# Kernel optimization log

Measured on AMD Instinct MI355X. Metric: run time of the kernel, lower is better.

Reference implementation:

```python
import jax, jax.numpy as jnp
import numpy as np

L_IN, L_K = 1, 1            # degree ranges (0..L)
C_IN, K_CH, H = 16, 8, 4    # in_channels, k_channels (per head), num_heads
C_OUT = H * K_CH            # 32
E, N_NODES, EMB = 32768, 4096, 64
M_IN, M_K = (L_IN + 1) ** 2, (L_K + 1) ** 2


def _so2_pairs(L_in, L_out):
    # enumerate SO(2)-equivariant weight blocks: for each order m, all (l_in, l_out)
    # pairs with l >= m; m=0 uses 1 matrix, m>0 uses 2 (real/imag parts).
    pairs, w = [], 0
    for m in range(min(L_in, L_out) + 1):
        for l_in in range(m, L_in + 1):
            for l_out in range(m, L_out + 1):
                pairs.append((m, l_in, l_out, w))
                w += 1 if m == 0 else 2
    return pairs, w

_PAIRS, NUM_W = _so2_pairs(L_IN, L_K)  # NUM_W = 6 for L_in=L_k=1


def so2_linear(x, W, L_in, L_out):
    # x: [E, (L_in+1)^2, Cin]; W: [NUM_W, Cin, Cout] (shared) or [E, NUM_W, Cin, Cout] (per-edge)
    per_edge = (W.ndim == 4)
    Cout = W.shape[-1]
    out = jnp.zeros((x.shape[0], (L_out + 1) ** 2, Cout), x.dtype)

    def mat(xs, w):
        return jnp.einsum('ec,eco->eo', xs, W[:, w]) if per_edge else xs @ W[w]

    pairs, _ = _so2_pairs(L_in, L_out)
    for m, l_in, l_out, w in pairs:
        i_in, i_out = l_in * (l_in + 1), l_out * (l_out + 1)  # flat index of (l, m=0)
        if m == 0:
            out = out.at[:, i_out].add(mat(x[:, i_in], w))
        else:
            xp, xn = x[:, i_in + m], x[:, i_in - m]
            out = out.at[:, i_out + m].add(mat(xp, w) - mat(xn, w + 1))
            out = out.at[:, i_out - m].add(mat(xp, w + 1) + mat(xn, w))
    return out


def segment_softmax(z, index, num_segments):
    # PyG-style softmax over ragged neighborhoods (max is detached, as in PyG)
    zmax = jax.lax.stop_gradient(jax.ops.segment_max(z, index, num_segments=num_segments))
    e = jnp.exp(z - zmax[index])
    denom = jax.ops.segment_sum(e, index, num_segments=num_segments)
    return e / denom[index]


def setup_inputs() -> dict:
    key = jax.random.key(0)
    ks = jax.random.split(key, 6)
    x_q = jax.random.normal(ks[0], (E, M_IN, C_IN), jnp.float32)
    x_k = jax.random.normal(ks[1], (E, M_IN, C_IN), jnp.float32)
    edge_emb = jax.random.normal(ks[2], (E, EMB), jnp.float32)
    index = jnp.sort(jax.random.randint(ks[3], (E,), 0, N_NODES))
    W_q = jax.random.normal(ks[4], (NUM_W, C_IN, C_OUT), jnp.float32) / np.sqrt(C_IN)
    W_p = jax.random.normal(ks[5], (EMB, NUM_W * C_IN * C_OUT), jnp.float32) / np.sqrt(EMB)
    return {"x_q": x_q, "x_k": x_k, "edge_emb": edge_emb, "index": index,
            "W_q": W_q, "W_p": W_p, "num_nodes": N_NODES}


def reference(x_q, x_k, edge_emb, index, W_q, W_p, num_nodes):
    # q_ij = W_Q x_i ; static SO2 weights
    q = so2_linear(x_q, W_q, L_IN, L_K).reshape(-1, M_K, H, K_CH)
    # k_ij = W_K(||r_ij||) x_j ; per-edge dynamic SO2 weights from edge embedding
    W_k = (edge_emb @ W_p).reshape(-1, NUM_W, C_IN, C_OUT)
    k = so2_linear(x_k, W_k, L_IN, L_K).reshape(-1, M_K, H, K_CH)
    scale = (K_CH // H) ** (-0.5)  # faithful to original: (k_channels // num_heads)**-0.5
    z = (q * k).sum((-1, -3)) * scale  # [E, H]
    return segment_softmax(z, index, num_nodes)
```

## Files before the change

### kernel.cpp

```cpp
#include <hip/hip_runtime.h>
#include <math.h>

#define E_TOTAL 32768
#define NUM_NODES 4096
#define SCALE 0.70710678118654752f

typedef __attribute__((ext_vector_type(8))) short bfrag;
typedef __attribute__((ext_vector_type(16))) float facc;

__device__ inline unsigned short f2bf(float f) {
  unsigned int u = __float_as_uint(f);
  unsigned int r = (u + 0x7FFFu + ((u >> 16) & 1u)) >> 16;
  return (unsigned short)r;
}
__device__ inline float bf2f(unsigned short s) {
  return __uint_as_float(((unsigned int)s) << 16);
}
__device__ inline void cvt8(const float* v, bfrag& hi, bfrag& lo) {
#pragma unroll
  for (int i = 0; i < 8; ++i) {
    unsigned short h = f2bf(v[i]);
    hi[i] = (short)h;
    lo[i] = (short)f2bf(v[i] - bf2f(h));
  }
}

__global__ __launch_bounds__(256) void prep_kernel(
    const float* __restrict__ Wp, const float* __restrict__ Wq,
    const int* __restrict__ index,
    unsigned short* __restrict__ fragWp, unsigned short* __restrict__ fragWq,
    int* __restrict__ offs)
{
  const int b = blockIdx.x, t = threadIdx.x;
  if (b < 96) {
    __shared__ unsigned short lds[4096];
    const int c = b / 6, w = b - c * 6;
    const int colbase = w * 512 + c * 32;
    const int cl = t & 31, dg = t >> 5;
#pragma unroll
    for (int i = 0; i < 8; ++i) {
      const int d = dg * 8 + i;
      const float v = Wp[(size_t)d * 3072 + colbase + cl];
      const unsigned short hi = f2bf(v);
      const unsigned short lo = f2bf(v - bf2f(hi));
      const int ks = d >> 4;
      const int lane = ((d >> 3) & 1) * 32 + cl;
      const int j = d & 7;
      lds[(ks * 2 + 0) * 512 + lane * 8 + j] = hi;
      lds[(ks * 2 + 1) * 512 + lane * 8 + j] = lo;
    }
    __syncthreads();
    unsigned short* dst = fragWp + (size_t)b * 4096;
    ((uint4*)dst)[t] = ((const uint4*)lds)[t];
    ((uint4*)dst)[t + 256] = ((const uint4*)lds)[t + 256];
  } else if (b < 103) {
    const int slot = b - 96;
    const int w = (slot == 6) ? 5 : slot;
    const float sgn = (slot == 6) ? -1.f : 1.f;
    for (int tt = t; tt < 512; tt += 256) {
      const int lane = tt >> 3, j = tt & 7;
      const int o = lane & 31, c = (lane >> 5) * 8 + j;
      const float v = sgn * Wq[(size_t)(w * 16 + c) * 32 + o];
      const unsigned short hi = f2bf(v);
      const unsigned short lo = f2bf(v - bf2f(hi));
      fragWq[slot * 1024 + lane * 8 + j] = hi;
      fragWq[slot * 1024 + 512 + lane * 8 + j] = lo;
    }
  } else {
    const int tg = (b - 103) * 256 + t;
    if (tg >= E_TOTAL) return;
    const int cur = index[tg];
    const int prev = (tg == 0) ? -1 : index[tg - 1];
    for (int n = prev + 1; n <= cur; ++n) offs[n] = tg;
    if (tg == E_TOTAL - 1)
      for (int n = cur + 1; n <= NUM_NODES; ++n) offs[n] = E_TOTAL;
  }
}

__global__ __launch_bounds__(256, 2) void main_kernel(
    const float* __restrict__ x_q, const float* __restrict__ x_k,
    const float* __restrict__ emb,
    const unsigned short* __restrict__ fragWp,
    const unsigned short* __restrict__ fragWq,
    float* __restrict__ z)
{
  __shared__ float xk_t[64][33];
  __shared__ float zred[4][32][4];

  const int t = threadIdx.x;
  const int lane = t & 63, wv = t >> 6;
  const int pr = wv & 1, ch = wv >> 1;
  const int col = lane & 31, half = lane >> 5;
  const int eb = blockIdx.x * 32;
  const int e = eb + col;

  {
    const int er = t >> 3, dq = (t & 7) * 8;
    const float* src = x_k + (size_t)(eb + er) * 64 + dq;
    float4 v0 = *(const float4*)(src);
    float4 v1 = *(const float4*)(src + 4);
    xk_t[dq + 0][er] = v0.x; xk_t[dq + 1][er] = v0.y;
    xk_t[dq + 2][er] = v0.z; xk_t[dq + 3][er] = v0.w;
    xk_t[dq + 4][er] = v1.x; xk_t[dq + 5][er] = v1.y;
    xk_t[dq + 6][er] = v1.z; xk_t[dq + 7][er] = v1.w;
  }

  bfrag ebh[4], ebl[4];
#pragma unroll
  for (int ks = 0; ks < 4; ++ks) {
    float tmp[8];
    *(float4*)&tmp[0] = *(const float4*)(emb + (size_t)e * 64 + ks * 16 + half * 8);
    *(float4*)&tmp[4] = *(const float4*)(emb + (size_t)e * 64 + ks * 16 + half * 8 + 4);
    cvt8(tmp, ebh[ks], ebl[ks]);
  }

  facc ka0 = {0}, ka1 = {0}, ka2 = {0}, ka3 = {0};

  const unsigned short* fbase = fragWp + lane * 8;

  bfrag curh[4], curl[4], nxth[4], nxtl[4];
  {
    const unsigned short* gp = fbase + (size_t)(ch * 6 + pr) * 4096;
#pragma unroll
    for (int ks = 0; ks < 4; ++ks) {
      *(uint4*)&curh[ks] = *(const uint4*)(gp + ks * 1024);
      *(uint4*)&curl[ks] = *(const uint4*)(gp + ks * 1024 + 512);
    }
  }

  __syncthreads();

  float xkc0 = 0.f, xkc1 = 0.f, xkc2 = 0.f, xkc3 = 0.f;

#pragma unroll 6
  for (int idx = 0; idx < 24; ++idx) {
    const int j = idx % 3;
    {
      const int nidx = (idx < 23) ? idx + 1 : 23;
      const int nc = ch + 2 * (nidx / 3);
      const int nw = pr + 2 * (nidx - 3 * (nidx / 3));
      const unsigned short* gp = fbase + (size_t)(nc * 6 + nw) * 4096;
#pragma unroll
      for (int ks = 0; ks < 4; ++ks) {
        *(uint4*)&nxth[ks] = *(const uint4*)(gp + ks * 1024);
        *(uint4*)&nxtl[ks] = *(const uint4*)(gp + ks * 1024 + 512);
      }
    }
    if (j == 0) {
      const int c = ch + 2 * (idx / 3);
      xkc0 = xk_t[c][col];
      xkc1 = xk_t[16 + c][col];
      xkc2 = xk_t[32 + c][col];
      xkc3 = xk_t[48 + c][col];
    }
    facc cc0 = {0.f}, cc1 = {0.f}, cc2 = {0.f};
#pragma unroll
    for (int ks = 0; ks < 4; ++ks) {
      cc0 = __builtin_amdgcn_mfma_f32_32x32x16_bf16(curh[ks], ebh[ks], cc0, 0, 0, 0);
      cc1 = __builtin_amdgcn_mfma_f32_32x32x16_bf16(curh[ks], ebl[ks], cc1, 0, 0, 0);
      cc2 = __builtin_amdgcn_mfma_f32_32x32x16_bf16(curl[ks], ebh[ks], cc2, 0, 0, 0);
    }
    if (j < 2) {
      const float xv = (j == 0) ? xkc0 : xkc2;
      if (pr == 0) {
#pragma unroll
        for (int r = 0; r < 16; ++r)
          ka0[r] = fmaf(xv, cc0[r] + cc1[r] + cc2[r], ka0[r]);
      } else {
#pragma unroll
        for (int r = 0; r < 16; ++r)
          ka2[r] = fmaf(xv, cc0[r] + cc1[r] + cc2[r], ka2[r]);
      }
    } else {
      if (pr == 0) {
#pragma unroll
        for (int r = 0; r < 16; ++r) {
          const float s = cc0[r] + cc1[r] + cc2[r];
          ka1[r] = fmaf(xkc1, s, ka1[r]);
          ka3[r] = fmaf(xkc3, s, ka3[r]);
        }
      } else {
#pragma unroll
        for (int r = 0; r < 16; ++r) {
          const float s = cc0[r] + cc1[r] + cc2[r];
          ka1[r] = fmaf(xkc3, s, ka1[r]);
          ka3[r] = fmaf(-xkc1, s, ka3[r]);
        }
      }
    }
#pragma unroll
    for (int ks = 0; ks < 4; ++ks) { curh[ks] = nxth[ks]; curl[ks] = nxtl[ks]; }
  }

  bfrag xqh[4], xql[4];
#pragma unroll
  for (int a = 0; a < 4; ++a) {
    float tmp[8];
    *(float4*)&tmp[0] = *(const float4*)(x_q + (size_t)e * 64 + a * 16 + half * 8);
    *(float4*)&tmp[4] = *(const float4*)(x_q + (size_t)e * 64 + a * 16 + half * 8 + 4);
    cvt8(tmp, xqh[a], xql[a]);
  }
  float zp0 = 0.f, zp1 = 0.f, zp2 = 0.f, zp3 = 0.f;
  const int QA1[4] = {0, 1, 0, 3}, QS1[4] = {0, 4, 1, 4};
  const int QA2[4] = {2, 3, 2, 1}, QS2[4] = {2, 5, 3, 6};
#pragma unroll
  for (int m = 0; m < 4; ++m) {
    facc qa = {0.f};
#pragma unroll
    for (int tm = 0; tm < 2; ++tm) {
      const int a = tm ? QA2[m] : QA1[m];
      const int sl = tm ? QS2[m] : QS1[m];
      bfrag wh, wl;
      *(uint4*)&wh = *(const uint4*)(fragWq + sl * 1024 + lane * 8);
      *(uint4*)&wl = *(const uint4*)(fragWq + sl * 1024 + 512 + lane * 8);
      qa = __builtin_amdgcn_mfma_f32_32x32x16_bf16(wh, xqh[a], qa, 0, 0, 0);
      qa = __builtin_amdgcn_mfma_f32_32x32x16_bf16(wh, xql[a], qa, 0, 0, 0);
      qa = __builtin_amdgcn_mfma_f32_32x32x16_bf16(wl, xqh[a], qa, 0, 0, 0);
    }
    const facc& km = (m == 0) ? ka0 : (m == 1) ? ka1 : (m == 2) ? ka2 : ka3;
#pragma unroll
    for (int r = 0; r < 16; ++r) {
      const float v = qa[r] * km[r];
      if (r < 4) zp0 += v;
      else if (r < 8) zp1 += v;
      else if (r < 12) zp2 += v;
      else zp3 += v;
    }
  }
  zp0 += __shfl_xor(zp0, 32);
  zp1 += __shfl_xor(zp1, 32);
  zp2 += __shfl_xor(zp2, 32);
  zp3 += __shfl_xor(zp3, 32);
  if (half == 0) {
    float4 v = {zp0, zp1, zp2, zp3};
    *(float4*)&zred[wv][col][0] = v;
  }
  __syncthreads();
  if (wv == 0 && half == 0) {
    float4 a = *(const float4*)&zred[0][col][0];
    float4 b = *(const float4*)&zred[1][col][0];
    float4 c4 = *(const float4*)&zred[2][col][0];
    float4 d4 = *(const float4*)&zred[3][col][0];
    float4 o = {(a.x + b.x + c4.x + d4.x) * SCALE,
                (a.y + b.y + c4.y + d4.y) * SCALE,
                (a.z + b.z + c4.z + d4.z) * SCALE,
                (a.w + b.w + c4.w + d4.w) * SCALE};
    *(float4*)&z[(size_t)e * 4] = o;
  }
}

__global__ __launch_bounds__(256) void softmax_kernel(
    const float* __restrict__ z, const int* __restrict__ offs,
    float* __restrict__ out)
{
  const int node = blockIdx.x * 4 + (threadIdx.x >> 6);
  const int lane = threadIdx.x & 63;
  const int start = offs[node], end = offs[node + 1];
  if (start >= end) return;
  const int h = lane & 3, eo = lane >> 2;
  float m = -INFINITY;
  for (int e = start + eo; e < end; e += 16) m = fmaxf(m, z[(size_t)e * 4 + h]);
#pragma unroll
  for (int s = 4; s < 64; s <<= 1) m = fmaxf(m, __shfl_xor(m, s));
  float sum = 0.f;
  for (int e = start + eo; e < end; e += 16) sum += __expf(z[(size_t)e * 4 + h] - m);
#pragma unroll
  for (int s = 4; s < 64; s <<= 1) sum += __shfl_xor(sum, s);
  const float inv = 1.f / sum;
  for (int e = start + eo; e < end; e += 16)
    out[(size_t)e * 4 + h] = __expf(z[(size_t)e * 4 + h] - m) * inv;
}

extern "C" void kernel_launch(void* const* d_in, const int* in_sizes, int n_in,
                              void* d_out, int out_size, void* d_ws, size_t ws_size,
                              hipStream_t stream) {
  const float* x_q = (const float*)d_in[0];
  const float* x_k = (const float*)d_in[1];
  const float* emb = (const float*)d_in[2];
  const int* index = (const int*)d_in[3];
  const float* W_q = (const float*)d_in[4];
  const float* W_p = (const float*)d_in[5];
  float* out = (float*)d_out;

  char* ws = (char*)d_ws;
  float* z = (float*)ws;
  int* offs = (int*)(ws + 524288);
  unsigned short* fragWp = (unsigned short*)(ws + 524288 + 32768);
  unsigned short* fragWq = (unsigned short*)(ws + 524288 + 32768 + 786432);

  prep_kernel<<<231, 256, 0, stream>>>(W_p, W_q, index, fragWp, fragWq, offs);
  main_kernel<<<1024, 256, 0, stream>>>(x_q, x_k, emb, fragWp, fragWq, z);
  softmax_kernel<<<1024, 256, 0, stream>>>(z, offs, out);
}
```

Baseline: 126.0 us.

## Merge prep, main and softmax kernels into one cooperative persistent kernel

Replaces the three back-to-back launches with a single cooperative kernel. Grid-wide syncs separate the weight-fragment prep, the per-edge score computation and the segment softmax, and blocks loop persistently over work items. This removes two kernel launch boundaries and their idle gaps. In exchange it adds grid-sync cost, runs a fixed grid of 256 or 512 blocks that may lose some latency hiding, and adds LDS for the prep buffer, which could affect occupancy.

```diff
diff --git a/kernel.cpp b/kernel.cpp
--- a/kernel.cpp
+++ b/kernel.cpp
@@ -1,9 +1,12 @@
 #include <hip/hip_runtime.h>
+#include <hip/hip_cooperative_groups.h>
 #include <math.h>
 
 #define E_TOTAL 32768
 #define NUM_NODES 4096
 #define SCALE 0.70710678118654752f
+
+namespace cg = cooperative_groups;
 
 typedef __attribute__((ext_vector_type(8))) short bfrag;
 typedef __attribute__((ext_vector_type(16))) float facc;
@@ -25,65 +28,14 @@
   }
 }
 
-__global__ __launch_bounds__(256) void prep_kernel(
-    const float* __restrict__ Wp, const float* __restrict__ Wq,
-    const int* __restrict__ index,
+__global__ __launch_bounds__(256, 2) void mega_kernel(
+    const float* __restrict__ x_q, const float* __restrict__ x_k,
+    const float* __restrict__ emb, const int* __restrict__ index,
+    const float* __restrict__ Wq, const float* __restrict__ Wp,
     unsigned short* __restrict__ fragWp, unsigned short* __restrict__ fragWq,
-    int* __restrict__ offs)
+    int* __restrict__ offs, float* __restrict__ z, float* __restrict__ out)
 {
-  const int b = blockIdx.x, t = threadIdx.x;
-  if (b < 96) {
-    __shared__ unsigned short lds[4096];
-    const int c = b / 6, w = b - c * 6;
-    const int colbase = w * 512 + c * 32;
-    const int cl = t & 31, dg = t >> 5;
-#pragma unroll
-    for (int i = 0; i < 8; ++i) {
-      const int d = dg * 8 + i;
-      const float v = Wp[(size_t)d * 3072 + colbase + cl];
-      const unsigned short hi = f2bf(v);
-      const unsigned short lo = f2bf(v - bf2f(hi));
-      const int ks = d >> 4;
-      const int lane = ((d >> 3) & 1) * 32 + cl;
-      const int j = d & 7;
-      lds[(ks * 2 + 0) * 512 + lane * 8 + j] = hi;
-      lds[(ks * 2 + 1) * 512 + lane * 8 + j] = lo;
-    }
-    __syncthreads();
-    unsigned short* dst = fragWp + (size_t)b * 4096;
-    ((uint4*)dst)[t] = ((const uint4*)lds)[t];
-    ((uint4*)dst)[t + 256] = ((const uint4*)lds)[t + 256];
-  } else if (b < 103) {
-    const int slot = b - 96;
-    const int w = (slot == 6) ? 5 : slot;
-    const float sgn = (slot == 6) ? -1.f : 1.f;
-    for (int tt = t; tt < 512; tt += 256) {
-      const int lane = tt >> 3, j = tt & 7;
-      const int o = lane & 31, c = (lane >> 5) * 8 + j;
-      const float v = sgn * Wq[(size_t)(w * 16 + c) * 32 + o];
-      const unsigned short hi = f2bf(v);
-      const unsigned short lo = f2bf(v - bf2f(hi));
-      fragWq[slot * 1024 + lane * 8 + j] = hi;
-      fragWq[slot * 1024 + 512 + lane * 8 + j] = lo;
-    }
-  } else {
-    const int tg = (b - 103) * 256 + t;
-    if (tg >= E_TOTAL) return;
-    const int cur = index[tg];
-    const int prev = (tg == 0) ? -1 : index[tg - 1];
-    for (int n = prev + 1; n <= cur; ++n) offs[n] = tg;
-    if (tg == E_TOTAL - 1)
-      for (int n = cur + 1; n <= NUM_NODES; ++n) offs[n] = E_TOTAL;
-  }
-}
-
-__global__ __launch_bounds__(256, 2) void main_kernel(
-    const float* __restrict__ x_q, const float* __restrict__ x_k,
-    const float* __restrict__ emb,
-    const unsigned short* __restrict__ fragWp,
-    const unsigned short* __restrict__ fragWq,
-    float* __restrict__ z)
-{
+  __shared__ unsigned short plds[4096];
   __shared__ float xk_t[64][33];
   __shared__ float zred[4][32][4];
 
@@ -91,184 +43,236 @@
   const int lane = t & 63, wv = t >> 6;
   const int pr = wv & 1, ch = wv >> 1;
   const int col = lane & 31, half = lane >> 5;
-  const int eb = blockIdx.x * 32;
-  const int e = eb + col;
-
-  {
-    const int er = t >> 3, dq = (t & 7) * 8;
-    const float* src = x_k + (size_t)(eb + er) * 64 + dq;
-    float4 v0 = *(const float4*)(src);
-    float4 v1 = *(const float4*)(src + 4);
-    xk_t[dq + 0][er] = v0.x; xk_t[dq + 1][er] = v0.y;
-    xk_t[dq + 2][er] = v0.z; xk_t[dq + 3][er] = v0.w;
-    xk_t[dq + 4][er] = v1.x; xk_t[dq + 5][er] = v1.y;
-    xk_t[dq + 6][er] = v1.z; xk_t[dq + 7][er] = v1.w;
+
+  for (int b = blockIdx.x; b < 231; b += gridDim.x) {
+    if (b < 96) {
+      const int c = b / 6, w = b - c * 6;
+      const int colbase = w * 512 + c * 32;
+      const int cl = t & 31, dg = t >> 5;
+#pragma unroll
+      for (int i = 0; i < 8; ++i) {
+        const int d = dg * 8 + i;
+        const float v = Wp[(size_t)d * 3072 + colbase + cl];
+        const unsigned short hi = f2bf(v);
+        const unsigned short lo = f2bf(v - bf2f(hi));
+        const int ks = d >> 4;
+        const int ln = ((d >> 3) & 1) * 32 + cl;
+        const int j = d & 7;
+        plds[(ks * 2 + 0) * 512 + ln * 8 + j] = hi;
+        plds[(ks * 2 + 1) * 512 + ln * 8 + j] = lo;
+      }
+      __syncthreads();
+      unsigned short* dst = fragWp + (size_t)b * 4096;
+      ((uint4*)dst)[t] = ((const uint4*)plds)[t];
+      ((uint4*)dst)[t + 256] = ((const uint4*)plds)[t + 256];
+      __syncthreads();
+    } else if (b < 103) {
+      const int slot = b - 96;
+      const int w = (slot == 6) ? 5 : slot;
+      const float sgn = (slot == 6) ? -1.f : 1.f;
+      for (int tt = t; tt < 512; tt += 256) {
+        const int ln = tt >> 3, j = tt & 7;
+        const int o = ln & 31, c = (ln >> 5) * 8 + j;
+        const float v = sgn * Wq[(size_t)(w * 16 + c) * 32 + o];
+        const unsigned short hi = f2bf(v);
+        const unsigned short lo = f2bf(v - bf2f(hi));
+        fragWq[slot * 1024 + ln * 8 + j] = hi;
+        fragWq[slot * 1024 + 512 + ln * 8 + j] = lo;
+      }
+    } else {
+      const int tg = (b - 103) * 256 + t;
+      if (tg < E_TOTAL) {
+        const int cur = index[tg];
+        const int prev = (tg == 0) ? -1 : index[tg - 1];
+        for (int n = prev + 1; n <= cur; ++n) offs[n] = tg;
+        if (tg == E_TOTAL - 1)
+          for (int n = cur + 1; n <= NUM_NODES; ++n) offs[n] = E_TOTAL;
+      }
+    }
   }
 
-  bfrag ebh[4], ebl[4];
-#pragma unroll
-  for (int ks = 0; ks < 4; ++ks) {
-    float tmp[8];
-    *(float4*)&tmp[0] = *(const float4*)(emb + (size_t)e * 64 + ks * 16 + half * 8);
-    *(float4*)&tmp[4] = *(const float4*)(emb + (size_t)e * 64 + ks * 16 + half * 8 + 4);
-    cvt8(tmp, ebh[ks], ebl[ks]);
-  }
-
-  facc ka0 = {0}, ka1 = {0}, ka2 = {0}, ka3 = {0};
-
-  const unsigned short* fbase = fragWp + lane * 8;
-
-  bfrag curh[4], curl[4], nxth[4], nxtl[4];
-  {
-    const unsigned short* gp = fbase + (size_t)(ch * 6 + pr) * 4096;
+  __threadfence();
+  cg::this_grid().sync();
+
+  for (int g = blockIdx.x; g < 1024; g += gridDim.x) {
+    const int eb = g * 32;
+    const int e = eb + col;
+
+    {
+      const int er = t >> 3, dq = (t & 7) * 8;
+      const float* src = x_k + (size_t)(eb + er) * 64 + dq;
+      float4 v0 = *(const float4*)(src);
+      float4 v1 = *(const float4*)(src + 4);
+      xk_t[dq + 0][er] = v0.x; xk_t[dq + 1][er] = v0.y;
+      xk_t[dq + 2][er] = v0.z; xk_t[dq + 3][er] = v0.w;
+      xk_t[dq + 4][er] = v1.x; xk_t[dq + 5][er] = v1.y;
+      xk_t[dq + 6][er] = v1.z; xk_t[dq + 7][er] = v1.w;
+    }
+
+    bfrag ebh[4], ebl[4];
 #pragma unroll
     for (int ks = 0; ks < 4; ++ks) {
-      *(uint4*)&curh[ks] = *(const uint4*)(gp + ks * 1024);
-      *(uint4*)&curl[ks] = *(const uint4*)(gp + ks * 1024 + 512);
-    }
-  }
-
-  __syncthreads();
-
-  float xkc0 = 0.f, xkc1 = 0.f, xkc2 = 0.f, xkc3 = 0.f;
+      float tmp[8];
+      *(float4*)&tmp[0] = *(const float4*)(emb + (size_t)e * 64 + ks * 16 + half * 8);
+      *(float4*)&tmp[4] = *(const float4*)(emb + (size_t)e * 64 + ks * 16 + half * 8 + 4);
+      cvt8(tmp, ebh[ks], ebl[ks]);
+    }
+
+    facc ka0 = {0}, ka1 = {0}, ka2 = {0}, ka3 = {0};
+    const unsigned short* fbase = fragWp + lane * 8;
+
+    bfrag curh[4], curl[4], nxth[4], nxtl[4];
+    {
+      const unsigned short* gp = fbase + (size_t)(ch * 6 + pr) * 4096;
+#pragma unroll
+      for (int ks = 0; ks < 4; ++ks) {
+        *(uint4*)&curh[ks] = *(const uint4*)(gp + ks * 1024);
+        *(uint4*)&curl[ks] = *(const uint4*)(gp + ks * 1024 + 512);
+      }
+    }
+
+    __syncthreads();
+
+    float xkc0 = 0.f, xkc1 = 0.f, xkc2 = 0.f, xkc3 = 0.f;
 
 #pragma unroll 6
-  for (int idx = 0; idx < 24; ++idx) {
-    const int j = idx % 3;
-    {
-      const int nidx = (idx < 23) ? idx + 1 : 23;
-      const int nc = ch + 2 * (nidx / 3);
-      const int nw = pr + 2 * (nidx - 3 * (nidx / 3));
-      const unsigned short* gp = fbase + (size_t)(nc * 6 + nw) * 4096;
+    for (int idx = 0; idx < 24; ++idx) {
+      const int j = idx % 3;
+      {
+        const int nidx = (idx < 23) ? idx + 1 : 23;
+        const int nc = ch + 2 * (nidx / 3);
+        const int nw = pr + 2 * (nidx - 3 * (nidx / 3));
+        const unsigned short* gp = fbase + (size_t)(nc * 6 + nw) * 4096;
+#pragma unroll
+        for (int ks = 0; ks < 4; ++ks) {
+          *(uint4*)&nxth[ks] = *(const uint4*)(gp + ks * 1024);
+          *(uint4*)&nxtl[ks] = *(const uint4*)(gp + ks * 1024 + 512);
+        }
+      }
+      if (j == 0) {
+        const int c = ch + 2 * (idx / 3);
+        xkc0 = xk_t[c][col];
+        xkc1 = xk_t[16 + c][col];
+        xkc2 = xk_t[32 + c][col];
+        xkc3 = xk_t[48 + c][col];
+      }
+      facc cc0 = {0.f}, cc1 = {0.f}, cc2 = {0.f};
 #pragma unroll
       for (int ks = 0; ks < 4; ++ks) {
-        *(uint4*)&nxth[ks] = *(const uint4*)(gp + ks * 1024);
-        *(uint4*)&nxtl[ks] = *(const uint4*)(gp + ks * 1024 + 512);
-      }
-    }
-    if (j == 0) {
-      const int c = ch + 2 * (idx / 3);
-      xkc0 = xk_t[c][col];
-      xkc1 = xk_t[16 + c][col];
-      xkc2 = xk_t[32 + c][col];
-      xkc3 = xk_t[48 + c][col];
-    }
-    facc cc0 = {0.f}, cc1 = {0.f}, cc2 = {0.f};
-#pragma unroll
-    for (int ks = 0; ks < 4; ++ks) {
-      cc0 = __builtin_amdgcn_mfma_f32_32x32x16_bf16(curh[ks], ebh[ks], cc0, 0, 0, 0);
-      cc1 = __builtin_amdgcn_mfma_f32_32x32x16_bf16(curh[ks], ebl[ks], cc1, 0, 0, 0);
-      cc2 = __builtin_amdgcn_mfma_f32_32x32x16_bf16(curl[ks], ebh[ks], cc2, 0, 0, 0);
-    }
-    if (j < 2) {
-      const float xv = (j == 0) ? xkc0 : xkc2;
-      if (pr == 0) {
-#pragma unroll
-        for (int r = 0; r < 16; ++r)
-          ka0[r] = fmaf(xv, cc0[r] + cc1[r] + cc2[r], ka0[r]);
-      } else {
-#pragma unroll
-        for (int r = 0; r < 16; ++r)
-          ka2[r] = fmaf(xv, cc0[r] + cc1[r] + cc2[r], ka2[r]);
-      }
-    } else {
-      if (pr == 0) {
-#pragma unroll
-        for (int r = 0; r < 16; ++r) {
-          const float s = cc0[r] + cc1[r] + cc2[r];
-          ka1[r] = fmaf(xkc1, s, ka1[r]);
-          ka3[r] = fmaf(xkc3, s, ka3[r]);
+        cc0 = __builtin_amdgcn_mfma_f32_32x32x16_bf16(curh[ks], ebh[ks], cc0, 0, 0, 0);
+        cc1 = __builtin_amdgcn_mfma_f32_32x32x16_bf16(curh[ks], ebl[ks], cc1, 0, 0, 0);
+        cc2 = __builtin_amdgcn_mfma_f32_32x32x16_bf16(curl[ks], ebh[ks], cc2, 0, 0, 0);
+      }
+      if (j < 2) {
+        const float xv = (j == 0) ? xkc0 : xkc2;
+        if (pr == 0) {
+#pragma unroll
+          for (int r = 0; r < 16; ++r)
+            ka0[r] = fmaf(xv, cc0[r] + cc1[r] + cc2[r], ka0[r]);
+        } else {
+#pragma unroll
+          for (int r = 0; r < 16; ++r)
+            ka2[r] = fmaf(xv, cc0[r] + cc1[r] + cc2[r], ka2[r]);
         }
       } else {
-#pragma unroll
-        for (int r = 0; r < 16; ++r) {
-          const float s = cc0[r] + cc1[r] + cc2[r];
-          ka1[r] = fmaf(xkc3, s, ka1[r]);
-          ka3[r] = fmaf(-xkc1, s, ka3[r]);
+        if (pr == 0) {
+#pragma unroll
+          for (int r = 0; r < 16; ++r) {
+            const float s = cc0[r] + cc1[r] + cc2[r];
+            ka1[r] = fmaf(xkc1, s, ka1[r]);
+            ka3[r] = fmaf(xkc3, s, ka3[r]);
+          }
+        } else {
+#pragma unroll
+          for (int r = 0; r < 16; ++r) {
+            const float s = cc0[r] + cc1[r] + cc2[r];
+            ka1[r] = fmaf(xkc3, s, ka1[r]);
+            ka3[r] = fmaf(-xkc1, s, ka3[r]);
+          }
         }
       }
-    }
-#pragma unroll
-    for (int ks = 0; ks < 4; ++ks) { curh[ks] = nxth[ks]; curl[ks] = nxtl[ks]; }
+#pragma unroll
+      for (int ks = 0; ks < 4; ++ks) { curh[ks] = nxth[ks]; curl[ks] = nxtl[ks]; }
+    }
+
+    bfrag xqh[4], xql[4];
+#pragma unroll
+    for (int a = 0; a < 4; ++a) {
+      float tmp[8];
+      *(float4*)&tmp[0] = *(const float4*)(x_q + (size_t)e * 64 + a * 16 + half * 8);
+      *(float4*)&tmp[4] = *(const float4*)(x_q + (size_t)e * 64 + a * 16 + half * 8 + 4);
+      cvt8(tmp, xqh[a], xql[a]);
+    }
+    float zp0 = 0.f, zp1 = 0.f, zp2 = 0.f, zp3 = 0.f;
+    const int QA1[4] = {0, 1, 0, 3}, QS1[4] = {0, 4, 1, 4};
+    const int QA2[4] = {2, 3, 2, 1}, QS2[4] = {2, 5, 3, 6};
+#pragma unroll
+    for (int m = 0; m < 4; ++m) {
+      facc qa = {0.f};
+#pragma unroll
+      for (int tm = 0; tm < 2; ++tm) {
+        const int a = tm ? QA2[m] : QA1[m];
+        const int sl = tm ? QS2[m] : QS1[m];
+        bfrag wh, wl;
+        *(uint4*)&wh = *(const uint4*)(fragWq + sl * 1024 + lane * 8);
+        *(uint4*)&wl = *(const uint4*)(fragWq + sl * 1024 + 512 + lane * 8);
+        qa = __builtin_amdgcn_mfma_f32_32x32x16_bf16(wh, xqh[a], qa, 0, 0, 0);
+        qa = __builtin_amdgcn_mfma_f32_32x32x16_bf16(wh, xql[a], qa, 0, 0, 0);
+        qa = __builtin_amdgcn_mfma_f32_32x32x16_bf16(wl, xqh[a], qa, 0, 0, 0);
+      }
+      const facc& km = (m == 0) ? ka0 : (m == 1) ? ka1 : (m == 2) ? ka2 : ka3;
+#pragma unroll
+      for (int r = 0; r < 16; ++r) {
+        const float v = qa[r] * km[r];
+        if (r < 4) zp0 += v;
+        else if (r < 8) zp1 += v;
+        else if (r < 12) zp2 += v;
+        else zp3 += v;
+      }
+    }
+    zp0 += __shfl_xor(zp0, 32);
+    zp1 += __shfl_xor(zp1, 32);
+    zp2 += __shfl_xor(zp2, 32);
+    zp3 += __shfl_xor(zp3, 32);
+    if (half == 0) {
+      float4 v = {zp0, zp1, zp2, zp3};
+      *(float4*)&zred[wv][col][0] = v;
+    }
+    __syncthreads();
+    if (wv == 0 && half == 0) {
+      float4 a = *(const float4*)&zred[0][col][0];
+      float4 b = *(const float4*)&zred[1][col][0];
+      float4 c4 = *(const float4*)&zred[2][col][0];
+      float4 d4 = *(const float4*)&zred[3][col][0];
+      float4 o = {(a.x + b.x + c4.x + d4.x) * SCALE,
+                  (a.y + b.y + c4.y + d4.y) * SCALE,
+                  (a.z + b.z + c4.z + d4.z) * SCALE,
+                  (a.w + b.w + c4.w + d4.w) * SCALE};
+      *(float4*)&z[(size_t)e * 4] = o;
+    }
   }
 
-  bfrag xqh[4], xql[4];
-#pragma unroll
-  for (int a = 0; a < 4; ++a) {
-    float tmp[8];
-    *(float4*)&tmp[0] = *(const float4*)(x_q + (size_t)e * 64 + a * 16 + half * 8);
-    *(float4*)&tmp[4] = *(const float4*)(x_q + (size_t)e * 64 + a * 16 + half * 8 + 4);
-    cvt8(tmp, xqh[a], xql[a]);
+  __threadfence();
+  cg::this_grid().sync();
+
+  for (int nb = blockIdx.x; nb < 1024; nb += gridDim.x) {
+    const int node = nb * 4 + wv;
+    const int start = offs[node], end = offs[node + 1];
+    if (start < end) {
+      const int h = lane & 3, eo = lane >> 2;
+      float m = -INFINITY;
+      for (int ee = start + eo; ee < end; ee += 16) m = fmaxf(m, z[(size_t)ee * 4 + h]);
+#pragma unroll
+      for (int s = 4; s < 64; s <<= 1) m = fmaxf(m, __shfl_xor(m, s));
+      float sum = 0.f;
+      for (int ee = start + eo; ee < end; ee += 16) sum += __expf(z[(size_t)ee * 4 + h] - m);
+#pragma unroll
+      for (int s = 4; s < 64; s <<= 1) sum += __shfl_xor(sum, s);
+      const float inv = 1.f / sum;
+      for (int ee = start + eo; ee < end; ee += 16)
+        out[(size_t)ee * 4 + h] = __expf(z[(size_t)ee * 4 + h] - m) * inv;
+    }
   }
-  float zp0 = 0.f, zp1 = 0.f, zp2 = 0.f, zp3 = 0.f;
-  const int QA1[4] = {0, 1, 0, 3}, QS1[4] = {0, 4, 1, 4};
-  const int QA2[4] = {2, 3, 2, 1}, QS2[4] = {2, 5, 3, 6};
-#pragma unroll
-  for (int m = 0; m < 4; ++m) {
-    facc qa = {0.f};
-#pragma unroll
-    for (int tm = 0; tm < 2; ++tm) {
-      const int a = tm ? QA2[m] : QA1[m];
-      const int sl = tm ? QS2[m] : QS1[m];
-      bfrag wh, wl;
-      *(uint4*)&wh = *(const uint4*)(fragWq + sl * 1024 + lane * 8);
-      *(uint4*)&wl = *(const uint4*)(fragWq + sl * 1024 + 512 + lane * 8);
-      qa = __builtin_amdgcn_mfma_f32_32x32x16_bf16(wh, xqh[a], qa, 0, 0, 0);
-      qa = __builtin_amdgcn_mfma_f32_32x32x16_bf16(wh, xql[a], qa, 0, 0, 0);
-      qa = __builtin_amdgcn_mfma_f32_32x32x16_bf16(wl, xqh[a], qa, 0, 0, 0);
-    }
-    const facc& km = (m == 0) ? ka0 : (m == 1) ? ka1 : (m == 2) ? ka2 : ka3;
-#pragma unroll
-    for (int r = 0; r < 16; ++r) {
-      const float v = qa[r] * km[r];
-      if (r < 4) zp0 += v;
-      else if (r < 8) zp1 += v;
-      else if (r < 12) zp2 += v;
-      else zp3 += v;
-    }
-  }
-  zp0 += __shfl_xor(zp0, 32);
-  zp1 += __shfl_xor(zp1, 32);
-  zp2 += __shfl_xor(zp2, 32);
-  zp3 += __shfl_xor(zp3, 32);
-  if (half == 0) {
-    float4 v = {zp0, zp1, zp2, zp3};
-    *(float4*)&zred[wv][col][0] = v;
-  }
-  __syncthreads();
-  if (wv == 0 && half == 0) {
-    float4 a = *(const float4*)&zred[0][col][0];
-    float4 b = *(const float4*)&zred[1][col][0];
-    float4 c4 = *(const float4*)&zred[2][col][0];
-    float4 d4 = *(const float4*)&zred[3][col][0];
-    float4 o = {(a.x + b.x + c4.x + d4.x) * SCALE,
-                (a.y + b.y + c4.y + d4.y) * SCALE,
-                (a.z + b.z + c4.z + d4.z) * SCALE,
-                (a.w + b.w + c4.w + d4.w) * SCALE};
-    *(float4*)&z[(size_t)e * 4] = o;
-  }
-}
-
-__global__ __launch_bounds__(256) void softmax_kernel(
-    const float* __restrict__ z, const int* __restrict__ offs,
-    float* __restrict__ out)
-{
-  const int node = blockIdx.x * 4 + (threadIdx.x >> 6);
-  const int lane = threadIdx.x & 63;
-  const int start = offs[node], end = offs[node + 1];
-  if (start >= end) return;
-  const int h = lane & 3, eo = lane >> 2;
-  float m = -INFINITY;
-  for (int e = start + eo; e < end; e += 16) m = fmaxf(m, z[(size_t)e * 4 + h]);
-#pragma unroll
-  for (int s = 4; s < 64; s <<= 1) m = fmaxf(m, __shfl_xor(m, s));
-  float sum = 0.f;
-  for (int e = start + eo; e < end; e += 16) sum += __expf(z[(size_t)e * 4 + h] - m);
-#pragma unroll
-  for (int s = 4; s < 64; s <<= 1) sum += __shfl_xor(sum, s);
-  const float inv = 1.f / sum;
-  for (int e = start + eo; e < end; e += 16)
-    out[(size_t)e * 4 + h] = __expf(z[(size_t)e * 4 + h] - m) * inv;
 }
 
 extern "C" void kernel_launch(void* const* d_in, const int* in_sizes, int n_in,
@@ -288,7 +292,13 @@
   unsigned short* fragWp = (unsigned short*)(ws + 524288 + 32768);
   unsigned short* fragWq = (unsigned short*)(ws + 524288 + 32768 + 786432);
 
-  prep_kernel<<<231, 256, 0, stream>>>(W_p, W_q, index, fragWp, fragWq, offs);
-  main_kernel<<<1024, 256, 0, stream>>>(x_q, x_k, emb, fragWp, fragWq, z);
-  softmax_kernel<<<1024, 256, 0, stream>>>(z, offs, out);
-}
+  int maxb = 0;
+  hipOccupancyMaxActiveBlocksPerMultiprocessor(&maxb, mega_kernel, 256, 0);
+  const int grid = (maxb >= 2) ? 512 : 256;
+
+  void* args[] = {(void*)&x_q, (void*)&x_k, (void*)&emb, (void*)&index,
+                  (void*)&W_q, (void*)&W_p, (void*)&fragWp, (void*)&fragWq,
+                  (void*)&offs, (void*)&z, (void*)&out};
+  hipLaunchCooperativeKernel((void*)mega_kernel, dim3(grid), dim3(256),
+                             args, 0, stream);
+}
```

Measured after the change: 257.4 us. 104% more time.
